# Kernel optimization log

Measured on AMD Instinct MI355X. Metric: run time of the kernel, lower is better.

## Reference

```python
import jax, jax.numpy as jnp
import numpy as np

D = 4096

def setup_inputs() -> dict:
    key = jax.random.key(0)
    k1, k2 = jax.random.split(key)
    matrix = jax.random.normal(k1, (D, D), dtype=jnp.float32)
    n = jax.random.normal(k2, (D,), dtype=jnp.float32)
    return {"matrix": matrix, "n": n}

def reference(matrix, n):
    # matrix @ matrix.T is PSD; adding a strictly positive softplus diagonal makes it SPD
    m = matrix @ matrix.T + jnp.diag(jax.nn.softplus(n))
    return jnp.linalg.cholesky(m)
```

## Files before the change

### kernel.cpp

```cpp
#include <hip/hip_runtime.h>
#include <math.h>

#define D 4096
#define NB 128
#define KC 32
#define NT (D / NB)
#define LDP 40

typedef __attribute__((ext_vector_type(8))) short short8;
typedef __attribute__((ext_vector_type(4))) float f32x4;
typedef __attribute__((ext_vector_type(4))) unsigned int uint4v;
typedef unsigned short ush;

__device__ __forceinline__ float softplusf(float x) {
  return fmaxf(x, 0.0f) + log1pf(expf(-fabsf(x)));
}

struct HL { unsigned int h, l; };

__device__ __forceinline__ HL split2(float x0, float x1) {
  unsigned int b0 = __float_as_uint(x0), b1 = __float_as_uint(x1);
  unsigned int h0 = b0 & 0xFFFF0000u, h1 = b1 & 0xFFFF0000u;
  float r0 = x0 - __uint_as_float(h0);
  float r1 = x1 - __uint_as_float(h1);
  HL out;
  out.h = h1 | (h0 >> 16);
  out.l = (__float_as_uint(r1) & 0xFFFF0000u) | (__float_as_uint(r0) >> 16);
  return out;
}

__device__ __forceinline__ void split1(float x, ush& h, ush& l) {
  unsigned int b = __float_as_uint(x);
  unsigned int hb = b & 0xFFFF0000u;
  float r = x - __uint_as_float(hb);
  h = (ush)(hb >> 16);
  l = (ush)(__float_as_uint(r) >> 16);
}

__device__ void potrf_factor(float (*Ls)[NB + 1]) {
  int tid = threadIdx.x;
  int lane = tid & 63, wid = tid >> 6;
  int tx = tid & 15, ty = tid >> 4;

  for (int pp = 0; pp < 8; ++pp) {
    int pc0 = pp * 16;
    if (wid == 0) {
      int ra = lane, rb = lane + 64;
      bool va = (ra >= pc0), vb = (rb >= pc0);
      float xa[16], xb[16];
#pragma unroll
      for (int c = 0; c < 16; ++c) {
        xa[c] = va ? Ls[ra][pc0 + c] : 0.0f;
        xb[c] = vb ? Ls[rb][pc0 + c] : 0.0f;
      }
#pragma unroll
      for (int j = 0; j < 16; ++j) {
        int jj = pc0 + j;
        float dv = (jj < 64) ? __shfl(xa[j], jj) : __shfl(xb[j], jj - 64);
        float di = __builtin_amdgcn_rcpf(dv);
        float ta = (ra > jj) ? xa[j] * di : 0.0f;
        float tb = (rb > jj) ? xb[j] * di : 0.0f;
#pragma unroll
        for (int c = j + 1; c < 16; ++c) {
          int rc = pc0 + c;
          float lc = (rc < 64) ? __shfl(xa[j], rc) : __shfl(xb[j], rc - 64);
          xa[c] -= ta * lc;
          xb[c] -= tb * lc;
        }
      }
#pragma unroll
      for (int c = 0; c < 16; ++c) {
        int rc = pc0 + c;
        float dc = (rc < 64) ? __shfl(xa[c], rc) : __shfl(xb[c], rc - 64);
        float sc = __builtin_amdgcn_rsqf(dc);
        xa[c] *= sc;
        xb[c] *= sc;
      }
      if (va) {
#pragma unroll
        for (int c = 0; c < 16; ++c) Ls[ra][pc0 + c] = xa[c];
      }
      if (vb) {
#pragma unroll
        for (int c = 0; c < 16; ++c) Ls[rb][pc0 + c] = xb[c];
      }
    }
    __syncthreads();

    int s0 = pc0 + 16;
    if (s0 < NB) {
      int r0 = ty * 8, c0 = tx * 8;
      if (r0 >= s0 && c0 >= s0) {
        float acc[8][8];
#pragma unroll
        for (int rr = 0; rr < 8; ++rr) {
          float4 m0 = *(const float4*)&Ls[r0 + rr][c0];
          float4 m1 = *(const float4*)&Ls[r0 + rr][c0 + 4];
          acc[rr][0] = m0.x; acc[rr][1] = m0.y; acc[rr][2] = m0.z; acc[rr][3] = m0.w;
          acc[rr][4] = m1.x; acc[rr][5] = m1.y; acc[rr][6] = m1.z; acc[rr][7] = m1.w;
        }
#pragma unroll
        for (int q = 0; q < 16; ++q) {
          float av[8], bv[8];
#pragma unroll
          for (int rr = 0; rr < 8; ++rr) av[rr] = Ls[r0 + rr][pc0 + q];
#pragma unroll
          for (int cc = 0; cc < 8; ++cc) bv[cc] = Ls[c0 + cc][pc0 + q];
#pragma unroll
          for (int rr = 0; rr < 8; ++rr)
#pragma unroll
            for (int cc = 0; cc < 8; ++cc) acc[rr][cc] -= av[rr] * bv[cc];
        }
#pragma unroll
        for (int rr = 0; rr < 8; ++rr) {
          *(float4*)&Ls[r0 + rr][c0] =
              make_float4(acc[rr][0], acc[rr][1], acc[rr][2], acc[rr][3]);
          *(float4*)&Ls[r0 + rr][c0 + 4] =
              make_float4(acc[rr][4], acc[rr][5], acc[rr][6], acc[rr][7]);
        }
      }
    }
    __syncthreads();
  }
}

__device__ void potrf_store(float* Msrc, float (*Ls)[NB + 1]) {
  int tid = threadIdx.x;
  for (int idx = tid; idx < NB * NB; idx += 256) {
    int i = idx >> 7, j = idx & (NB - 1);
    Msrc[(size_t)i * D + j] = (j <= i) ? Ls[i][j] : 0.0f;
  }
}

__global__ __launch_bounds__(256) void potrf_kernel(float* __restrict__ M, int kb)
{
  __shared__ float Ls[NB][NB + 1];
  int tid = threadIdx.x;
  float* Msrc = M + (size_t)kb * D + kb;
  for (int idx = tid; idx < NB * NB; idx += 256) {
    int i = idx >> 7, j = idx & (NB - 1);
    Ls[i][j] = Msrc[(size_t)i * D + j];
  }
  __syncthreads();
  potrf_factor(Ls);
  potrf_store(Msrc, Ls);
}

__global__ __launch_bounds__(256) void convA_kernel(
    const float* __restrict__ A, ush* __restrict__ AhG, ush* __restrict__ AlG)
{
  size_t idx = ((size_t)blockIdx.x * 256 + threadIdx.x) * 8;
  float4 v0 = *(const float4*)(A + idx);
  float4 v1 = *(const float4*)(A + idx + 4);
  HL p0 = split2(v0.x, v0.y), p1 = split2(v0.z, v0.w);
  HL p2 = split2(v1.x, v1.y), p3 = split2(v1.z, v1.w);
  uint4v h = {p0.h, p1.h, p2.h, p3.h};
  uint4v l = {p0.l, p1.l, p2.l, p3.l};
  *(uint4v*)(AhG + idx) = h;
  *(uint4v*)(AlG + idx) = l;
}

template <bool SHA>
__global__ __launch_bounds__(256) void syrk0_kernel(
    const float* __restrict__ Asrc, const float* __restrict__ nvec,
    float* __restrict__ Mout,
    const ush* __restrict__ AhG, const ush* __restrict__ AlG)
{
  __shared__ ush Ah[NB][LDP], Al[NB][LDP];
  __shared__ ush Bh[NB][LDP], Bl[NB][LDP];

  int b = blockIdx.x;
  int ti = (int)((sqrtf(8.0f * (float)b + 1.0f) - 1.0f) * 0.5f);
  while ((ti + 1) * (ti + 2) / 2 <= b) ++ti;
  while (ti * (ti + 1) / 2 > b) --ti;
  int tj = b - ti * (ti + 1) / 2;
  int row0 = ti * NB, col0 = tj * NB;

  int tid = threadIdx.x;
  int lane = tid & 63, wid = tid >> 6;
  int wr = wid >> 1, wc = wid & 1;
  int srow = tid >> 1;
  int scg = (tid & 1) * 16;

  f32x4 acc[4][4];
#pragma unroll
  for (int m = 0; m < 4; ++m)
#pragma unroll
    for (int n = 0; n < 4; ++n) acc[m][n] = (f32x4){0.f, 0.f, 0.f, 0.f};

  int lr16 = lane & 15, kof = (lane >> 4) * 8;

  for (int kk = 0; kk < D; kk += KC) {
    if (SHA) {
      const ush* pah = AhG + (size_t)(row0 + srow) * D + kk + scg;
      const ush* pal = AlG + (size_t)(row0 + srow) * D + kk + scg;
      const ush* pbh = AhG + (size_t)(col0 + srow) * D + kk + scg;
      const ush* pbl = AlG + (size_t)(col0 + srow) * D + kk + scg;
      short8 ah0 = *(const short8*)pah, ah1 = *(const short8*)(pah + 8);
      short8 al0 = *(const short8*)pal, al1 = *(const short8*)(pal + 8);
      short8 bh0 = *(const short8*)pbh, bh1 = *(const short8*)(pbh + 8);
      short8 bl0 = *(const short8*)pbl, bl1 = *(const short8*)(pbl + 8);
      __syncthreads();
      *(short8*)&Ah[srow][scg] = ah0;  *(short8*)&Ah[srow][scg + 8] = ah1;
      *(short8*)&Al[srow][scg] = al0;  *(short8*)&Al[srow][scg + 8] = al1;
      *(short8*)&Bh[srow][scg] = bh0;  *(short8*)&Bh[srow][scg + 8] = bh1;
      *(short8*)&Bl[srow][scg] = bl0;  *(short8*)&Bl[srow][scg + 8] = bl1;
    } else {
      const float* pa = Asrc + (size_t)(row0 + srow) * D + kk + scg;
      const float* pb = Asrc + (size_t)(col0 + srow) * D + kk + scg;
      float4 av0 = *(const float4*)(pa + 0), av1 = *(const float4*)(pa + 4);
      float4 av2 = *(const float4*)(pa + 8), av3 = *(const float4*)(pa + 12);
      float4 bv0 = *(const float4*)(pb + 0), bv1 = *(const float4*)(pb + 4);
      float4 bv2 = *(const float4*)(pb + 8), bv3 = *(const float4*)(pb + 12);
      __syncthreads();
      {
        HL p0 = split2(av0.x, av0.y), p1 = split2(av0.z, av0.w);
        HL p2 = split2(av1.x, av1.y), p3 = split2(av1.z, av1.w);
        HL p4 = split2(av2.x, av2.y), p5 = split2(av2.z, av2.w);
        HL p6 = split2(av3.x, av3.y), p7 = split2(av3.z, av3.w);
        uint4v h0 = {p0.h, p1.h, p2.h, p3.h}, l0 = {p0.l, p1.l, p2.l, p3.l};
        uint4v h1 = {p4.h, p5.h, p6.h, p7.h}, l1 = {p4.l, p5.l, p6.l, p7.l};
        *(uint4v*)&Ah[srow][scg] = h0;  *(uint4v*)&Ah[srow][scg + 8] = h1;
        *(uint4v*)&Al[srow][scg] = l0;  *(uint4v*)&Al[srow][scg + 8] = l1;
      }
      {
        HL p0 = split2(bv0.x, bv0.y), p1 = split2(bv0.z, bv0.w);
        HL p2 = split2(bv1.x, bv1.y), p3 = split2(bv1.z, bv1.w);
        HL p4 = split2(bv2.x, bv2.y), p5 = split2(bv2.z, bv2.w);
        HL p6 = split2(bv3.x, bv3.y), p7 = split2(bv3.z, bv3.w);
        uint4v h0 = {p0.h, p1.h, p2.h, p3.h}, l0 = {p0.l, p1.l, p2.l, p3.l};
        uint4v h1 = {p4.h, p5.h, p6.h, p7.h}, l1 = {p4.l, p5.l, p6.l, p7.l};
        *(uint4v*)&Bh[srow][scg] = h0;  *(uint4v*)&Bh[srow][scg + 8] = h1;
        *(uint4v*)&Bl[srow][scg] = l0;  *(uint4v*)&Bl[srow][scg + 8] = l1;
      }
    }
    __syncthreads();

    short8 ah[4], al[4], bh[4], bl[4];
#pragma unroll
    for (int m = 0; m < 4; ++m) {
      int r = wr * 64 + m * 16 + lr16;
      ah[m] = *(const short8*)&Ah[r][kof];
      al[m] = *(const short8*)&Al[r][kof];
    }
#pragma unroll
    for (int n = 0; n < 4; ++n) {
      int c = wc * 64 + n * 16 + lr16;
      bh[n] = *(const short8*)&Bh[c][kof];
      bl[n] = *(const short8*)&Bl[c][kof];
    }
#pragma unroll
    for (int m = 0; m < 4; ++m)
#pragma unroll
      for (int n = 0; n < 4; ++n) {
        acc[m][n] = __builtin_amdgcn_mfma_f32_16x16x32_bf16(ah[m], bh[n], acc[m][n], 0, 0, 0);
        acc[m][n] = __builtin_amdgcn_mfma_f32_16x16x32_bf16(ah[m], bl[n], acc[m][n], 0, 0, 0);
        acc[m][n] = __builtin_amdgcn_mfma_f32_16x16x32_bf16(al[m], bh[n], acc[m][n], 0, 0, 0);
      }
  }

  int cl = lane & 15, rg = (lane >> 4) * 4;
#pragma unroll
  for (int m = 0; m < 4; ++m) {
#pragma unroll
    for (int n = 0; n < 4; ++n) {
      int gi0 = row0 + wr * 64 + m * 16 + rg;
      int gj = col0 + wc * 64 + n * 16 + cl;
#pragma unroll
      for (int r = 0; r < 4; ++r) {
        int gi = gi0 + r;
        float v = acc[m][n][r];
        if (gi == gj) v += softplusf(nvec[gi]);
        Mout[(size_t)gi * D + gj] = v;
      }
    }
  }

  if (ti > tj) {
    float4 z = make_float4(0.f, 0.f, 0.f, 0.f);
    int zr = tid >> 1;
    int zc0 = (tid & 1) * 64;
    float* zp = Mout + (size_t)(col0 + zr) * D + row0 + zc0;
#pragma unroll
    for (int q = 0; q < 16; ++q) *(float4*)(zp + 4 * q) = z;
  }
}

template <bool SH>
__global__ __launch_bounds__(256) void trsm_kernel(
    float* __restrict__ M, int kb, ush* __restrict__ shH, ush* __restrict__ shL)
{
  __shared__ float Ls[NB][NB + 1];
  __shared__ float dinv[NB];
  int tid = threadIdx.x;
  const float* Lsrc = M + (size_t)kb * D + kb;
  for (int idx = tid; idx < NB * NB; idx += 256) {
    int i = idx >> 7, j = idx & (NB - 1);
    Ls[i][j] = Lsrc[(size_t)i * D + j];
  }
  __syncthreads();
  if (tid < NB) dinv[tid] = 1.0f / Ls[tid][tid];
  __syncthreads();
  int lane = tid & 63, w = tid >> 6;
  size_t r0 = (size_t)(kb + NB) + (size_t)blockIdx.x * 8 + w * 2;
  float* p0 = M + r0 * D + kb;
  float* p1 = p0 + D;
  float x0l = p0[lane], x0h = p0[64 + lane];
  float x1l = p1[lane], x1h = p1[64 + lane];
  for (int p = 0; p < 64; ++p) {
    float dv = dinv[p];
    float xp0 = __shfl(x0l, p) * dv;
    float xp1 = __shfl(x1l, p) * dv;
    float Llo = Ls[lane][p];
    float Lhi = Ls[64 + lane][p];
    if (lane == p)      { x0l = xp0; x1l = xp1; }
    else if (lane > p)  { x0l -= xp0 * Llo; x1l -= xp1 * Llo; }
    x0h -= xp0 * Lhi;
    x1h -= xp1 * Lhi;
  }
  for (int p = 64; p < NB; ++p) {
    int q = p - 64;
    float dv = dinv[p];
    float xp0 = __shfl(x0h, q) * dv;
    float xp1 = __shfl(x1h, q) * dv;
    float Lhi = Ls[64 + lane][p];
    if (lane == q)      { x0h = xp0; x1h = xp1; }
    else if (lane > q)  { x0h -= xp0 * Lhi; x1h -= xp1 * Lhi; }
  }
  p0[lane] = x0l; p0[64 + lane] = x0h;
  p1[lane] = x1l; p1[64 + lane] = x1h;
  if (SH) {
    ush h, l;
    split1(x0l, h, l);
    shH[r0 * NB + lane] = h;        shL[r0 * NB + lane] = l;
    split1(x0h, h, l);
    shH[r0 * NB + 64 + lane] = h;   shL[r0 * NB + 64 + lane] = l;
    split1(x1l, h, l);
    shH[(r0 + 1) * NB + lane] = h;      shL[(r0 + 1) * NB + lane] = l;
    split1(x1h, h, l);
    shH[(r0 + 1) * NB + 64 + lane] = h; shL[(r0 + 1) * NB + 64 + lane] = l;
  }
}

__device__ void gemm_bt(const float* __restrict__ Ap, const float* __restrict__ Bp,
                        f32x4 (&acc)[4][4],
                        ush (*Ah)[LDP], ush (*Al)[LDP],
                        ush (*Bh)[LDP], ush (*Bl)[LDP])
{
  int tid = threadIdx.x;
  int lane = tid & 63, wid = tid >> 6;
  int wr = wid >> 1, wc = wid & 1;
  int srow = tid >> 1, scg = (tid & 1) * 16;
  int lr16 = lane & 15, kof = (lane >> 4) * 8;

  for (int kk = 0; kk < NB; kk += KC) {
    const float* pa = Ap + (size_t)srow * D + kk + scg;
    const float* pb = Bp + (size_t)srow * D + kk + scg;
    float4 av0 = *(const float4*)(pa + 0), av1 = *(const float4*)(pa + 4);
    float4 av2 = *(const float4*)(pa + 8), av3 = *(const float4*)(pa + 12);
    float4 bv0 = *(const float4*)(pb + 0), bv1 = *(const float4*)(pb + 4);
    float4 bv2 = *(const float4*)(pb + 8), bv3 = *(const float4*)(pb + 12);

    __syncthreads();
    {
      HL p0 = split2(av0.x, av0.y), p1 = split2(av0.z, av0.w);
      HL p2 = split2(av1.x, av1.y), p3 = split2(av1.z, av1.w);
      HL p4 = split2(av2.x, av2.y), p5 = split2(av2.z, av2.w);
      HL p6 = split2(av3.x, av3.y), p7 = split2(av3.z, av3.w);
      uint4v h0 = {p0.h, p1.h, p2.h, p3.h}, l0 = {p0.l, p1.l, p2.l, p3.l};
      uint4v h1 = {p4.h, p5.h, p6.h, p7.h}, l1 = {p4.l, p5.l, p6.l, p7.l};
      *(uint4v*)&Ah[srow][scg] = h0;  *(uint4v*)&Ah[srow][scg + 8] = h1;
      *(uint4v*)&Al[srow][scg] = l0;  *(uint4v*)&Al[srow][scg + 8] = l1;
    }
    {
      HL p0 = split2(bv0.x, bv0.y), p1 = split2(bv0.z, bv0.w);
      HL p2 = split2(bv1.x, bv1.y), p3 = split2(bv1.z, bv1.w);
      HL p4 = split2(bv2.x, bv2.y), p5 = split2(bv2.z, bv2.w);
      HL p6 = split2(bv3.x, bv3.y), p7 = split2(bv3.z, bv3.w);
      uint4v h0 = {p0.h, p1.h, p2.h, p3.h}, l0 = {p0.l, p1.l, p2.l, p3.l};
      uint4v h1 = {p4.h, p5.h, p6.h, p7.h}, l1 = {p4.l, p5.l, p6.l, p7.l};
      *(uint4v*)&Bh[srow][scg] = h0;  *(uint4v*)&Bh[srow][scg + 8] = h1;
      *(uint4v*)&Bl[srow][scg] = l0;  *(uint4v*)&Bl[srow][scg + 8] = l1;
    }
    __syncthreads();

    short8 ah[4], al[4], bh[4], bl[4];
#pragma unroll
    for (int m = 0; m < 4; ++m) {
      int r = wr * 64 + m * 16 + lr16;
      ah[m] = *(const short8*)&Ah[r][kof];
      al[m] = *(const short8*)&Al[r][kof];
    }
#pragma unroll
    for (int n = 0; n < 4; ++n) {
      int c = wc * 64 + n * 16 + lr16;
      bh[n] = *(const short8*)&Bh[c][kof];
      bl[n] = *(const short8*)&Bl[c][kof];
    }
#pragma unroll
    for (int m = 0; m < 4; ++m)
#pragma unroll
      for (int n = 0; n < 4; ++n) {
        acc[m][n] = __builtin_amdgcn_mfma_f32_16x16x32_bf16(ah[m], bh[n], acc[m][n], 0, 0, 0);
        acc[m][n] = __builtin_amdgcn_mfma_f32_16x16x32_bf16(ah[m], bl[n], acc[m][n], 0, 0, 0);
        acc[m][n] = __builtin_amdgcn_mfma_f32_16x16x32_bf16(al[m], bh[n], acc[m][n], 0, 0, 0);
      }
  }
}

__device__ void gemm_bt_sh(const ush* __restrict__ AhG, const ush* __restrict__ AlG,
                           const ush* __restrict__ BhG, const ush* __restrict__ BlG,
                           f32x4 (&acc)[4][4],
                           ush (*Ah)[LDP], ush (*Al)[LDP],
                           ush (*Bh)[LDP], ush (*Bl)[LDP])
{
  int tid = threadIdx.x;
  int lane = tid & 63, wid = tid >> 6;
  int wr = wid >> 1, wc = wid & 1;
  int srow = tid >> 1, scg = (tid & 1) * 16;
  int lr16 = lane & 15, kof = (lane >> 4) * 8;

  for (int kk = 0; kk < NB; kk += KC) {
    const ush* pah = AhG + (size_t)srow * NB + kk + scg;
    const ush* pal = AlG + (size_t)srow * NB + kk + scg;
    const ush* pbh = BhG + (size_t)srow * NB + kk + scg;
    const ush* pbl = BlG + (size_t)srow * NB + kk + scg;
    short8 vah0 = *(const short8*)(pah), vah1 = *(const short8*)(pah + 8);
    short8 val0 = *(const short8*)(pal), val1 = *(const short8*)(pal + 8);
    short8 vbh0 = *(const short8*)(pbh), vbh1 = *(const short8*)(pbh + 8);
    short8 vbl0 = *(const short8*)(pbl), vbl1 = *(const short8*)(pbl + 8);

    __syncthreads();
    *(short8*)&Ah[srow][scg] = vah0;  *(short8*)&Ah[srow][scg + 8] = vah1;
    *(short8*)&Al[srow][scg] = val0;  *(short8*)&Al[srow][scg + 8] = val1;
    *(short8*)&Bh[srow][scg] = vbh0;  *(short8*)&Bh[srow][scg + 8] = vbh1;
    *(short8*)&Bl[srow][scg] = vbl0;  *(short8*)&Bl[srow][scg + 8] = vbl1;
    __syncthreads();

    short8 ah[4], al[4], bh[4], bl[4];
#pragma unroll
    for (int m = 0; m < 4; ++m) {
      int r = wr * 64 + m * 16 + lr16;
      ah[m] = *(const short8*)&Ah[r][kof];
      al[m] = *(const short8*)&Al[r][kof];
    }
#pragma unroll
    for (int n = 0; n < 4; ++n) {
      int c = wc * 64 + n * 16 + lr16;
      bh[n] = *(const short8*)&Bh[c][kof];
      bl[n] = *(const short8*)&Bl[c][kof];
    }
#pragma unroll
    for (int m = 0; m < 4; ++m)
#pragma unroll
      for (int n = 0; n < 4; ++n) {
        acc[m][n] = __builtin_amdgcn_mfma_f32_16x16x32_bf16(ah[m], bh[n], acc[m][n], 0, 0, 0);
        acc[m][n] = __builtin_amdgcn_mfma_f32_16x16x32_bf16(ah[m], bl[n], acc[m][n], 0, 0, 0);
        acc[m][n] = __builtin_amdgcn_mfma_f32_16x16x32_bf16(al[m], bh[n], acc[m][n], 0, 0, 0);
      }
  }
}

__global__ __launch_bounds__(256) void panel_update_kernel(
    float* __restrict__ M, int k, int pend,
    const ush* __restrict__ shH, const ush* __restrict__ shL)
{
  __shared__ __align__(16) unsigned char smem[66560];
  ush (*Ah)[LDP] = (ush(*)[LDP])(smem);
  ush (*Al)[LDP] = (ush(*)[LDP])(smem + 10240);
  ush (*Bh)[LDP] = (ush(*)[LDP])(smem + 20480);
  ush (*Bl)[LDP] = (ush(*)[LDP])(smem + 30720);
  float (*Ls)[NB + 1] = (float(*)[NB + 1])smem;

  int s = blockIdx.x;
  int j = k + 1, rem = s;
  while (rem >= NT - j) { rem -= NT - j; ++j; }
  int i = j + rem;
  (void)pend;

  int tid = threadIdx.x;
  int lane = tid & 63, wid = tid >> 6;
  int wr = wid >> 1, wc = wid & 1;
  int cl = lane & 15, rg = (lane >> 4) * 4;

  f32x4 acc[4][4];
#pragma unroll
  for (int m = 0; m < 4; ++m)
#pragma unroll
    for (int n = 0; n < 4; ++n) acc[m][n] = (f32x4){0.f, 0.f, 0.f, 0.f};

  size_t ra = (size_t)(i * NB) * NB;
  size_t rb = (size_t)(j * NB) * NB;
  gemm_bt_sh(shH + ra, shL + ra, shH + rb, shL + rb, acc, Ah, Al, Bh, Bl);

  float* Mt = M + (size_t)(i * NB) * D + j * NB;
  if (s == 0) {
    __syncthreads();
#pragma unroll
    for (int m = 0; m < 4; ++m)
#pragma unroll
      for (int n = 0; n < 4; ++n) {
        int li0 = wr * 64 + m * 16 + rg;
        int lj = wc * 64 + n * 16 + cl;
#pragma unroll
        for (int r = 0; r < 4; ++r)
          Ls[li0 + r][lj] = Mt[(size_t)(li0 + r) * D + lj] - acc[m][n][r];
      }
    __syncthreads();
    potrf_factor(Ls);
    potrf_store(Mt, Ls);
    return;
  }
#pragma unroll
  for (int m = 0; m < 4; ++m)
#pragma unroll
    for (int n = 0; n < 4; ++n) {
      int li0 = wr * 64 + m * 16 + rg;
      int lj = wc * 64 + n * 16 + cl;
#pragma unroll
      for (int r = 0; r < 4; ++r)
        Mt[(size_t)(li0 + r) * D + lj] -= acc[m][n][r];
    }
}

__global__ __launch_bounds__(256) void syrk4_kernel(
    float* __restrict__ M, int base,
    const ush* __restrict__ h0, const ush* __restrict__ l0,
    const ush* __restrict__ h1, const ush* __restrict__ l1,
    const ush* __restrict__ h2, const ush* __restrict__ l2,
    const ush* __restrict__ h3, const ush* __restrict__ l3)
{
  __shared__ __align__(16) unsigned char smem[66560];
  ush (*Ah)[LDP] = (ush(*)[LDP])(smem);
  ush (*Al)[LDP] = (ush(*)[LDP])(smem + 10240);
  ush (*Bh)[LDP] = (ush(*)[LDP])(smem + 20480);
  ush (*Bl)[LDP] = (ush(*)[LDP])(smem + 30720);
  float (*Ls)[NB + 1] = (float(*)[NB + 1])smem;

  int s = blockIdx.x;
  int tp = (int)((sqrtf(8.0f * (float)s + 1.0f) - 1.0f) * 0.5f);
  while ((tp + 1) * (tp + 2) / 2 <= s) ++tp;
  while (tp * (tp + 1) / 2 > s) --tp;
  int tq = s - tp * (tp + 1) / 2;
  int i = base + tp, j = base + tq;

  int tid = threadIdx.x;
  int lane = tid & 63, wid = tid >> 6;
  int wr = wid >> 1, wc = wid & 1;
  int cl = lane & 15, rg = (lane >> 4) * 4;

  f32x4 acc[4][4];
#pragma unroll
  for (int m = 0; m < 4; ++m)
#pragma unroll
    for (int n = 0; n < 4; ++n) acc[m][n] = (f32x4){0.f, 0.f, 0.f, 0.f};

  size_t ra = (size_t)(i * NB) * NB;
  size_t rb = (size_t)(j * NB) * NB;
  gemm_bt_sh(h0 + ra, l0 + ra, h0 + rb, l0 + rb, acc, Ah, Al, Bh, Bl);
  gemm_bt_sh(h1 + ra, l1 + ra, h1 + rb, l1 + rb, acc, Ah, Al, Bh, Bl);
  gemm_bt_sh(h2 + ra, l2 + ra, h2 + rb, l2 + rb, acc, Ah, Al, Bh, Bl);
  gemm_bt_sh(h3 + ra, l3 + ra, h3 + rb, l3 + rb, acc, Ah, Al, Bh, Bl);

  float* Mt = M + (size_t)(i * NB) * D + j * NB;
  if (s == 0) {
    __syncthreads();
#pragma unroll
    for (int m = 0; m < 4; ++m)
#pragma unroll
      for (int n = 0; n < 4; ++n) {
        int li0 = wr * 64 + m * 16 + rg;
        int lj = wc * 64 + n * 16 + cl;
#pragma unroll
        for (int r = 0; r < 4; ++r)
          Ls[li0 + r][lj] = Mt[(size_t)(li0 + r) * D + lj] - acc[m][n][r];
      }
    __syncthreads();
    potrf_factor(Ls);
    potrf_store(Mt, Ls);
    return;
  }
#pragma unroll
  for (int m = 0; m < 4; ++m)
#pragma unroll
    for (int n = 0; n < 4; ++n) {
      int li0 = wr * 64 + m * 16 + rg;
      int lj = wc * 64 + n * 16 + cl;
#pragma unroll
      for (int r = 0; r < 4; ++r)
        Mt[(size_t)(li0 + r) * D + lj] -= acc[m][n][r];
    }
}

__global__ __launch_bounds__(256) void syrk1_fb_kernel(float* __restrict__ M, int kb)
{
  __shared__ __align__(16) unsigned char smem[66560];
  ush (*Ah)[LDP] = (ush(*)[LDP])(smem);
  ush (*Al)[LDP] = (ush(*)[LDP])(smem + 10240);
  ush (*Bh)[LDP] = (ush(*)[LDP])(smem + 20480);
  ush (*Bl)[LDP] = (ush(*)[LDP])(smem + 30720);
  float (*Ls)[NB + 1] = (float(*)[NB + 1])smem;

  float* Mout = M + (size_t)(kb + NB) * D + (kb + NB);
  const float* Xsrc = M + (size_t)(kb + NB) * D + kb;

  int s = blockIdx.x;
  int ti = (int)((sqrtf(8.0f * (float)s + 1.0f) - 1.0f) * 0.5f);
  while ((ti + 1) * (ti + 2) / 2 <= s) ++ti;
  while (ti * (ti + 1) / 2 > s) --ti;
  int tj = s - ti * (ti + 1) / 2;
  int row0 = ti * NB, col0 = tj * NB;

  int tid = threadIdx.x;
  int lane = tid & 63, wid = tid >> 6;
  int wr = wid >> 1, wc = wid & 1;
  int cl = lane & 15, rg = (lane >> 4) * 4;

  f32x4 acc[4][4];
#pragma unroll
  for (int m = 0; m < 4; ++m)
#pragma unroll
    for (int n = 0; n < 4; ++n) acc[m][n] = (f32x4){0.f, 0.f, 0.f, 0.f};

  gemm_bt(Xsrc + (size_t)row0 * D, Xsrc + (size_t)col0 * D, acc, Ah, Al, Bh, Bl);

  if (s == 0) {
    __syncthreads();
#pragma unroll
    for (int m = 0; m < 4; ++m)
#pragma unroll
      for (int n = 0; n < 4; ++n) {
        int li0 = wr * 64 + m * 16 + rg;
        int lj = wc * 64 + n * 16 + cl;
#pragma unroll
        for (int r = 0; r < 4; ++r)
          Ls[li0 + r][lj] = Mout[(size_t)(li0 + r) * D + lj] - acc[m][n][r];
      }
    __syncthreads();
    potrf_factor(Ls);
    potrf_store(Mout, Ls);
    return;
  }
#pragma unroll
  for (int m = 0; m < 4; ++m)
#pragma unroll
    for (int n = 0; n < 4; ++n) {
      int gi0 = row0 + wr * 64 + m * 16 + rg;
      int gj = col0 + wc * 64 + n * 16 + cl;
#pragma unroll
      for (int r = 0; r < 4; ++r)
        Mout[(size_t)(gi0 + r) * D + gj] -= acc[m][n][r];
    }
}

extern "C" void kernel_launch(void* const* d_in, const int* in_sizes, int n_in,
                              void* d_out, int out_size, void* d_ws, size_t ws_size,
                              hipStream_t stream)
{
  (void)in_sizes; (void)n_in; (void)out_size;
  const float* A  = (const float*)d_in[0];
  const float* nv = (const float*)d_in[1];
  float* M = (float*)d_out;

  const size_t ash_elems = (size_t)D * D;
  const size_t bank = (size_t)D * NB;
  const size_t need = 2 * ash_elems * sizeof(ush);
  bool shA = (ws_size >= need);
  ush* aH = (ush*)d_ws;
  ush* aL = aH + ash_elems;
  ush* bk[8];
  for (int q = 0; q < 8; ++q) bk[q] = (ush*)d_ws + q * bank;

  if (shA) {
    convA_kernel<<<(int)(ash_elems / 8 / 256), 256, 0, stream>>>(A, aH, aL);
    syrk0_kernel<true><<<NT * (NT + 1) / 2, 256, 0, stream>>>(A, nv, M, aH, aL);
    potrf_kernel<<<1, 256, 0, stream>>>(M, 0);

    for (int p = 0; p < 8; ++p) {
      int pend = 4 * p + 3;
      for (int q = 0; q < 4; ++q) {
        int k = 4 * p + q;
        if (k > 30) break;
        int T = D - k * NB - NB;
        trsm_kernel<true><<<T / 8, 256, 0, stream>>>(M, k * NB, bk[2 * q], bk[2 * q + 1]);
        if (q < 3) {
          int npu = 0;
          for (int j = k + 1; j <= pend; ++j) npu += NT - j;
          panel_update_kernel<<<npu, 256, 0, stream>>>(M, k, pend, bk[2 * q], bk[2 * q + 1]);
        }
      }
      if (p < 7) {
        int base = 4 * (p + 1);
        int t2 = NT - base;
        syrk4_kernel<<<t2 * (t2 + 1) / 2, 256, 0, stream>>>(
            M, base, bk[0], bk[1], bk[2], bk[3], bk[4], bk[5], bk[6], bk[7]);
      }
    }
  } else {
    syrk0_kernel<false><<<NT * (NT + 1) / 2, 256, 0, stream>>>(A, nv, M, nullptr, nullptr);
    potrf_kernel<<<1, 256, 0, stream>>>(M, 0);
    for (int k = 0; k <= 30; ++k) {
      int kb = k * NB;
      int T = D - kb - NB;
      int t = T / NB;
      trsm_kernel<false><<<T / 8, 256, 0, stream>>>(M, kb, nullptr, nullptr);
      syrk1_fb_kernel<<<t * (t + 1) / 2, 256, 0, stream>>>(M, kb);
    }
  }
}
```

Measured before the change: 3.753 ms.

## Fuse TRSM, lookahead panel factor and trailing SYRK into one step kernel

Replaces the blocked scheme of per-step TRSM launches, panel-update launches and a batched four-panel SYRK with one fused step kernel per column block, preceded by a single diag1 kernel for the first diagonal block. Each step launch carries three roles: blocks that lazily apply the previous panel's update to their rows and then solve the TRSM, one lookahead block that updates, solves and factors the next diagonal block, and blocks that apply the trailing rank-NB update from the previous panel. This cuts the number of kernel launches and overlaps the serial potrf and TRSM work with the trailing update, using two ping-pong bf16 split buffers. In exchange the trailing update is applied one panel at a time instead of four panels batched, and the single lookahead block does a long serial chain that can become the critical path.

```diff
diff --git a/kernel.cpp b/kernel.cpp
--- a/kernel.cpp
+++ b/kernel.cpp
@@ -461,9 +461,8 @@
   }
 }
 
-__global__ __launch_bounds__(256) void panel_update_kernel(
-    float* __restrict__ M, int k, int pend,
-    const ush* __restrict__ shH, const ush* __restrict__ shL)
+__global__ __launch_bounds__(256) void diag1_kernel(
+    float* __restrict__ M, const ush* __restrict__ bH, const ush* __restrict__ bL)
 {
   __shared__ __align__(16) unsigned char smem[66560];
   ush (*Ah)[LDP] = (ush(*)[LDP])(smem);
@@ -472,12 +471,6 @@
   ush (*Bl)[LDP] = (ush(*)[LDP])(smem + 30720);
   float (*Ls)[NB + 1] = (float(*)[NB + 1])smem;
 
-  int s = blockIdx.x;
-  int j = k + 1, rem = s;
-  while (rem >= NT - j) { rem -= NT - j; ++j; }
-  int i = j + rem;
-  (void)pend;
-
   int tid = threadIdx.x;
   int lane = tid & 63, wid = tid >> 6;
   int wr = wid >> 1, wc = wid & 1;
@@ -488,14 +481,126 @@
   for (int m = 0; m < 4; ++m)
 #pragma unroll
     for (int n = 0; n < 4; ++n) acc[m][n] = (f32x4){0.f, 0.f, 0.f, 0.f};
-
-  size_t ra = (size_t)(i * NB) * NB;
-  size_t rb = (size_t)(j * NB) * NB;
-  gemm_bt_sh(shH + ra, shL + ra, shH + rb, shL + rb, acc, Ah, Al, Bh, Bl);
-
-  float* Mt = M + (size_t)(i * NB) * D + j * NB;
-  if (s == 0) {
-    __syncthreads();
+  size_t ra = (size_t)NB * NB;
+  gemm_bt_sh(bH + ra, bL + ra, bH + ra, bL + ra, acc, Ah, Al, Bh, Bl);
+  __syncthreads();
+  float* Mt = M + (size_t)NB * D + NB;
+#pragma unroll
+  for (int m = 0; m < 4; ++m)
+#pragma unroll
+    for (int n = 0; n < 4; ++n) {
+      int li0 = wr * 64 + m * 16 + rg;
+      int lj = wc * 64 + n * 16 + cl;
+#pragma unroll
+      for (int r = 0; r < 4; ++r)
+        Ls[li0 + r][lj] = Mt[(size_t)(li0 + r) * D + lj] - acc[m][n][r];
+    }
+  __syncthreads();
+  potrf_factor(Ls);
+  potrf_store(Mt, Ls);
+}
+
+__global__ __launch_bounds__(256) void step_kernel(
+    float* __restrict__ M, int k,
+    const ush* __restrict__ phH, const ush* __restrict__ phL,
+    ush* __restrict__ pcH, ush* __restrict__ pcL)
+{
+  __shared__ __align__(16) unsigned char smem[70656];
+  int tid = threadIdx.x;
+  int lane = tid & 63, w = tid >> 6;
+  int t1 = NT - 1 - k;
+  int nT = (t1 >= 2) ? (t1 - 1) * (NB / 8) : 0;
+  int bid = blockIdx.x;
+
+  if (bid < nT) {
+    float (*XB)[NB + 1] = (float(*)[NB + 1])smem;
+    float (*XA)[NB] = (float(*)[NB])(smem + 66048);
+    size_t base = (size_t)(k + 2) * NB + (size_t)bid * 8;
+    float* p0 = M + (base + w * 2) * D + (size_t)k * NB;
+    float* p1 = p0 + D;
+    float x0l = p0[lane], x0h = p0[64 + lane];
+    float x1l = p1[lane], x1h = p1[64 + lane];
+    const float* Xk = M + (size_t)k * NB * D + (size_t)(k - 1) * NB;
+    for (int idx = tid; idx < NB * NB; idx += 256) {
+      int c = idx >> 7, p = idx & (NB - 1);
+      XB[p][c] = Xk[(size_t)c * D + p];
+    }
+    for (int idx = tid; idx < 8 * NB; idx += 256) {
+      int r = idx >> 7, p = idx & (NB - 1);
+      XA[r][p] = M[(base + r) * D + (size_t)(k - 1) * NB + p];
+    }
+    __syncthreads();
+    for (int p = 0; p < NB; ++p) {
+      float xa0 = XA[w * 2][p], xa1 = XA[w * 2 + 1][p];
+      float xb_lo = XB[p][lane], xb_hi = XB[p][64 + lane];
+      x0l -= xa0 * xb_lo; x0h -= xa0 * xb_hi;
+      x1l -= xa1 * xb_lo; x1h -= xa1 * xb_hi;
+    }
+    __syncthreads();
+    float (*Ls)[NB + 1] = (float(*)[NB + 1])smem;
+    float* dinv = (float*)(smem + 66048);
+    const float* Lsrc = M + (size_t)k * NB * D + (size_t)k * NB;
+    for (int idx = tid; idx < NB * NB; idx += 256) {
+      int i = idx >> 7, j = idx & (NB - 1);
+      Ls[i][j] = Lsrc[(size_t)i * D + j];
+    }
+    __syncthreads();
+    if (tid < NB) dinv[tid] = 1.0f / Ls[tid][tid];
+    __syncthreads();
+    for (int p = 0; p < 64; ++p) {
+      float dv = dinv[p];
+      float xp0 = __shfl(x0l, p) * dv;
+      float xp1 = __shfl(x1l, p) * dv;
+      float Llo = Ls[lane][p];
+      float Lhi = Ls[64 + lane][p];
+      if (lane == p)      { x0l = xp0; x1l = xp1; }
+      else if (lane > p)  { x0l -= xp0 * Llo; x1l -= xp1 * Llo; }
+      x0h -= xp0 * Lhi;
+      x1h -= xp1 * Lhi;
+    }
+    for (int p = 64; p < NB; ++p) {
+      int q = p - 64;
+      float dv = dinv[p];
+      float xp0 = __shfl(x0h, q) * dv;
+      float xp1 = __shfl(x1h, q) * dv;
+      float Lhi = Ls[64 + lane][p];
+      if (lane == q)      { x0h = xp0; x1h = xp1; }
+      else if (lane > q)  { x0h -= xp0 * Lhi; x1h -= xp1 * Lhi; }
+    }
+    p0[lane] = x0l; p0[64 + lane] = x0h;
+    p1[lane] = x1l; p1[64 + lane] = x1h;
+    size_t r0 = base + w * 2;
+    ush h, l;
+    split1(x0l, h, l);
+    pcH[r0 * NB + lane] = h;        pcL[r0 * NB + lane] = l;
+    split1(x0h, h, l);
+    pcH[r0 * NB + 64 + lane] = h;   pcL[r0 * NB + 64 + lane] = l;
+    split1(x1l, h, l);
+    pcH[(r0 + 1) * NB + lane] = h;      pcL[(r0 + 1) * NB + lane] = l;
+    split1(x1h, h, l);
+    pcH[(r0 + 1) * NB + 64 + lane] = h; pcL[(r0 + 1) * NB + 64 + lane] = l;
+    return;
+  }
+
+  ush (*Ah)[LDP] = (ush(*)[LDP])(smem);
+  ush (*Al)[LDP] = (ush(*)[LDP])(smem + 10240);
+  ush (*Bh)[LDP] = (ush(*)[LDP])(smem + 20480);
+  ush (*Bl)[LDP] = (ush(*)[LDP])(smem + 30720);
+  float (*Ls)[NB + 1] = (float(*)[NB + 1])smem;
+  float* dinv = (float*)(smem + 66048);
+  int wr = w >> 1, wc = w & 1;
+  int cl = lane & 15, rg = (lane >> 4) * 4;
+
+  if (bid == nT) {
+    int i1 = k + 1;
+    f32x4 acc[4][4];
+#pragma unroll
+    for (int m = 0; m < 4; ++m)
+#pragma unroll
+      for (int n = 0; n < 4; ++n) acc[m][n] = (f32x4){0.f, 0.f, 0.f, 0.f};
+    size_t ra = (size_t)i1 * NB * NB, rk = (size_t)k * NB * NB;
+    gemm_bt_sh(phH + ra, phL + ra, phH + rk, phL + rk, acc, Ah, Al, Bh, Bl);
+    float* Mt = M + (size_t)i1 * NB * D + (size_t)k * NB;
 #pragma unroll
     for (int m = 0; m < 4; ++m)
 #pragma unroll
@@ -504,13 +609,97 @@
         int lj = wc * 64 + n * 16 + cl;
 #pragma unroll
         for (int r = 0; r < 4; ++r)
-          Ls[li0 + r][lj] = Mt[(size_t)(li0 + r) * D + lj] - acc[m][n][r];
+          Mt[(size_t)(li0 + r) * D + lj] -= acc[m][n][r];
+      }
+    __syncthreads();
+    const float* Lsrc = M + (size_t)k * NB * D + (size_t)k * NB;
+    for (int idx = tid; idx < NB * NB; idx += 256) {
+      int i = idx >> 7, j = idx & (NB - 1);
+      Ls[i][j] = Lsrc[(size_t)i * D + j];
+    }
+    __syncthreads();
+    if (tid < NB) dinv[tid] = 1.0f / Ls[tid][tid];
+    __syncthreads();
+    for (int g = 0; g < 16; ++g) {
+      size_t r0 = (size_t)i1 * NB + g * 8 + w * 2;
+      float* q0 = M + r0 * D + (size_t)k * NB;
+      float* q1 = q0 + D;
+      float x0l = q0[lane], x0h = q0[64 + lane];
+      float x1l = q1[lane], x1h = q1[64 + lane];
+      for (int p = 0; p < 64; ++p) {
+        float dv = dinv[p];
+        float xp0 = __shfl(x0l, p) * dv;
+        float xp1 = __shfl(x1l, p) * dv;
+        float Llo = Ls[lane][p];
+        float Lhi = Ls[64 + lane][p];
+        if (lane == p)      { x0l = xp0; x1l = xp1; }
+        else if (lane > p)  { x0l -= xp0 * Llo; x1l -= xp1 * Llo; }
+        x0h -= xp0 * Lhi;
+        x1h -= xp1 * Lhi;
+      }
+      for (int p = 64; p < NB; ++p) {
+        int q = p - 64;
+        float dv = dinv[p];
+        float xp0 = __shfl(x0h, q) * dv;
+        float xp1 = __shfl(x1h, q) * dv;
+        float Lhi = Ls[64 + lane][p];
+        if (lane == q)      { x0h = xp0; x1h = xp1; }
+        else if (lane > q)  { x0h -= xp0 * Lhi; x1h -= xp1 * Lhi; }
+      }
+      q0[lane] = x0l; q0[64 + lane] = x0h;
+      q1[lane] = x1l; q1[64 + lane] = x1h;
+      ush h, l;
+      split1(x0l, h, l);
+      pcH[r0 * NB + lane] = h;        pcL[r0 * NB + lane] = l;
+      split1(x0h, h, l);
+      pcH[r0 * NB + 64 + lane] = h;   pcL[r0 * NB + 64 + lane] = l;
+      split1(x1l, h, l);
+      pcH[(r0 + 1) * NB + lane] = h;      pcL[(r0 + 1) * NB + lane] = l;
+      split1(x1h, h, l);
+      pcH[(r0 + 1) * NB + 64 + lane] = h; pcL[(r0 + 1) * NB + 64 + lane] = l;
+    }
+    __syncthreads();
+    f32x4 acc2[4][4];
+#pragma unroll
+    for (int m = 0; m < 4; ++m)
+#pragma unroll
+      for (int n = 0; n < 4; ++n) acc2[m][n] = (f32x4){0.f, 0.f, 0.f, 0.f};
+    gemm_bt_sh(pcH + ra, pcL + ra, pcH + ra, pcL + ra, acc2, Ah, Al, Bh, Bl);
+    gemm_bt_sh(phH + ra, phL + ra, phH + ra, phL + ra, acc2, Ah, Al, Bh, Bl);
+    __syncthreads();
+    float* Md = M + (size_t)i1 * NB * D + (size_t)i1 * NB;
+#pragma unroll
+    for (int m = 0; m < 4; ++m)
+#pragma unroll
+      for (int n = 0; n < 4; ++n) {
+        int li0 = wr * 64 + m * 16 + rg;
+        int lj = wc * 64 + n * 16 + cl;
+#pragma unroll
+        for (int r = 0; r < 4; ++r)
+          Ls[li0 + r][lj] = Md[(size_t)(li0 + r) * D + lj] - acc2[m][n][r];
       }
     __syncthreads();
     potrf_factor(Ls);
-    potrf_store(Mt, Ls);
+    potrf_store(Md, Ls);
     return;
   }
+
+  int s = bid - nT;
+  int tp = (int)((sqrtf(8.0f * (float)s + 1.0f) - 1.0f) * 0.5f);
+  while ((tp + 1) * (tp + 2) / 2 <= s) ++tp;
+  while (tp * (tp + 1) / 2 > s) --tp;
+  int tq = s - tp * (tp + 1) / 2;
+  int i = k + 1 + tp, j = k + 1 + tq;
+
+  f32x4 acc[4][4];
+#pragma unroll
+  for (int m = 0; m < 4; ++m)
+#pragma unroll
+    for (int n = 0; n < 4; ++n) acc[m][n] = (f32x4){0.f, 0.f, 0.f, 0.f};
+  size_t ra = (size_t)i * NB * NB, rb = (size_t)j * NB * NB;
+  gemm_bt_sh(phH + ra, phL + ra, phH + rb, phL + rb, acc, Ah, Al, Bh, Bl);
+
+  float* Mt = M + (size_t)i * NB * D + (size_t)j * NB;
 #pragma unroll
   for (int m = 0; m < 4; ++m)
 #pragma unroll
@@ -523,12 +712,7 @@
     }
 }
 
-__global__ __launch_bounds__(256) void syrk4_kernel(
-    float* __restrict__ M, int base,
-    const ush* __restrict__ h0, const ush* __restrict__ l0,
-    const ush* __restrict__ h1, const ush* __restrict__ l1,
-    const ush* __restrict__ h2, const ush* __restrict__ l2,
-    const ush* __restrict__ h3, const ush* __restrict__ l3)
+__global__ __launch_bounds__(256) void syrk1_fb_kernel(float* __restrict__ M, int kb)
 {
   __shared__ __align__(16) unsigned char smem[66560];
   ush (*Ah)[LDP] = (ush(*)[LDP])(smem);
@@ -537,70 +721,6 @@
   ush (*Bl)[LDP] = (ush(*)[LDP])(smem + 30720);
   float (*Ls)[NB + 1] = (float(*)[NB + 1])smem;
 
-  int s = blockIdx.x;
-  int tp = (int)((sqrtf(8.0f * (float)s + 1.0f) - 1.0f) * 0.5f);
-  while ((tp + 1) * (tp + 2) / 2 <= s) ++tp;
-  while (tp * (tp + 1) / 2 > s) --tp;
-  int tq = s - tp * (tp + 1) / 2;
-  int i = base + tp, j = base + tq;
-
-  int tid = threadIdx.x;
-  int lane = tid & 63, wid = tid >> 6;
-  int wr = wid >> 1, wc = wid & 1;
-  int cl = lane & 15, rg = (lane >> 4) * 4;
-
-  f32x4 acc[4][4];
-#pragma unroll
-  for (int m = 0; m < 4; ++m)
-#pragma unroll
-    for (int n = 0; n < 4; ++n) acc[m][n] = (f32x4){0.f, 0.f, 0.f, 0.f};
-
-  size_t ra = (size_t)(i * NB) * NB;
-  size_t rb = (size_t)(j * NB) * NB;
-  gemm_bt_sh(h0 + ra, l0 + ra, h0 + rb, l0 + rb, acc, Ah, Al, Bh, Bl);
-  gemm_bt_sh(h1 + ra, l1 + ra, h1 + rb, l1 + rb, acc, Ah, Al, Bh, Bl);
-  gemm_bt_sh(h2 + ra, l2 + ra, h2 + rb, l2 + rb, acc, Ah, Al, Bh, Bl);
-  gemm_bt_sh(h3 + ra, l3 + ra, h3 + rb, l3 + rb, acc, Ah, Al, Bh, Bl);
-
-  float* Mt = M + (size_t)(i * NB) * D + j * NB;
-  if (s == 0) {
-    __syncthreads();
-#pragma unroll
-    for (int m = 0; m < 4; ++m)
-#pragma unroll
-      for (int n = 0; n < 4; ++n) {
-        int li0 = wr * 64 + m * 16 + rg;
-        int lj = wc * 64 + n * 16 + cl;
-#pragma unroll
-        for (int r = 0; r < 4; ++r)
-          Ls[li0 + r][lj] = Mt[(size_t)(li0 + r) * D + lj] - acc[m][n][r];
-      }
-    __syncthreads();
-    potrf_factor(Ls);
-    potrf_store(Mt, Ls);
-    return;
-  }
-#pragma unroll
-  for (int m = 0; m < 4; ++m)
-#pragma unroll
-    for (int n = 0; n < 4; ++n) {
-      int li0 = wr * 64 + m * 16 + rg;
-      int lj = wc * 64 + n * 16 + cl;
-#pragma unroll
-      for (int r = 0; r < 4; ++r)
-        Mt[(size_t)(li0 + r) * D + lj] -= acc[m][n][r];
-    }
-}
-
-__global__ __launch_bounds__(256) void syrk1_fb_kernel(float* __restrict__ M, int kb)
-{
-  __shared__ __align__(16) unsigned char smem[66560];
-  ush (*Ah)[LDP] = (ush(*)[LDP])(smem);
-  ush (*Al)[LDP] = (ush(*)[LDP])(smem + 10240);
-  ush (*Bh)[LDP] = (ush(*)[LDP])(smem + 20480);
-  ush (*Bl)[LDP] = (ush(*)[LDP])(smem + 30720);
-  float (*Ls)[NB + 1] = (float(*)[NB + 1])smem;
-
   float* Mout = M + (size_t)(kb + NB) * D + (kb + NB);
   const float* Xsrc = M + (size_t)(kb + NB) * D + kb;
 
@@ -668,33 +788,28 @@
   bool shA = (ws_size >= need);
   ush* aH = (ush*)d_ws;
   ush* aL = aH + ash_elems;
-  ush* bk[8];
-  for (int q = 0; q < 8; ++q) bk[q] = (ush*)d_ws + q * bank;
+  ush* b0H = (ush*)d_ws;
+  ush* b0L = b0H + bank;
+  ush* b1H = b0L + bank;
+  ush* b1L = b1H + bank;
 
   if (shA) {
     convA_kernel<<<(int)(ash_elems / 8 / 256), 256, 0, stream>>>(A, aH, aL);
     syrk0_kernel<true><<<NT * (NT + 1) / 2, 256, 0, stream>>>(A, nv, M, aH, aL);
     potrf_kernel<<<1, 256, 0, stream>>>(M, 0);
-
-    for (int p = 0; p < 8; ++p) {
-      int pend = 4 * p + 3;
-      for (int q = 0; q < 4; ++q) {
-        int k = 4 * p + q;
-        if (k > 30) break;
-        int T = D - k * NB - NB;
-        trsm_kernel<true><<<T / 8, 256, 0, stream>>>(M, k * NB, bk[2 * q], bk[2 * q + 1]);
-        if (q < 3) {
-          int npu = 0;
-          for (int j = k + 1; j <= pend; ++j) npu += NT - j;
-          panel_update_kernel<<<npu, 256, 0, stream>>>(M, k, pend, bk[2 * q], bk[2 * q + 1]);
-        }
-      }
-      if (p < 7) {
-        int base = 4 * (p + 1);
-        int t2 = NT - base;
-        syrk4_kernel<<<t2 * (t2 + 1) / 2, 256, 0, stream>>>(
-            M, base, bk[0], bk[1], bk[2], bk[3], bk[4], bk[5], bk[6], bk[7]);
-      }
+    trsm_kernel<true><<<(D - NB) / 8, 256, 0, stream>>>(M, 0, b0H, b0L);
+    diag1_kernel<<<1, 256, 0, stream>>>(M, b0H, b0L);
+
+    for (int k = 1; k <= 30; ++k) {
+      int t1 = NT - 1 - k;
+      int nT = (t1 >= 2) ? (t1 - 1) * (NB / 8) : 0;
+      int P = t1 * (t1 + 1) / 2;
+      int grid = nT + P;
+      ush* phH = (k & 1) ? b0H : b1H;
+      ush* phL = (k & 1) ? b0L : b1L;
+      ush* pcH = (k & 1) ? b1H : b0H;
+      ush* pcL = (k & 1) ? b1L : b0L;
+      step_kernel<<<grid, 256, 0, stream>>>(M, k, phH, phL, pcH, pcL);
     }
   } else {
     syrk0_kernel<false><<<NT * (NT + 1) / 2, 256, 0, stream>>>(A, nv, M, nullptr, nullptr);
```

After: 9.313 ms. 2.48x slower.
